# Performance work log

Measured on AMD Instinct MI355X. Metric: run time of the kernel, lower is better.

## Reference

```python
import jax, jax.numpy as jnp
import numpy as np

B, T, D, H = 4, 2048, 1024, 16
HD = D // H
K = 4            # templates per token
VOCAB = 32000


def setup_inputs() -> dict:
    key = jax.random.key(0)
    ks = jax.random.split(key, 6)
    x = jax.random.normal(ks[0], (B, T, D), dtype=jnp.float32)
    sequences = jax.random.randint(ks[1], (B, T, K), 0, VOCAB, dtype=jnp.int64)
    # xavier-uniform-ish scaled weights (torch Linear stores [out, in])
    Wqkv = jax.random.normal(ks[2], (3 * D, D), dtype=jnp.float32) * (1.0 / np.sqrt(D))
    Wout = jax.random.normal(ks[3], (D, D), dtype=jnp.float32) * (1.0 / np.sqrt(D))
    bout = jnp.zeros((D,), dtype=jnp.float32)
    emb = jax.random.normal(ks[4], (VOCAB, D), dtype=jnp.float32) * 0.02
    bias_scale = jnp.asarray(0.1, dtype=jnp.float32)
    return {"x": x, "sequences": sequences, "Wqkv": Wqkv, "Wout": Wout,
            "bout": bout, "emb": emb, "bias_scale": bias_scale}


def reference(x, sequences, Wqkv, Wout, bout, emb, bias_scale):
    b, t, d = x.shape
    h, hd = H, d // H
    # qkv projection (no bias): [B,T,3,H,hd]
    qkv = (x @ Wqkv.T).reshape(b, t, 3, h, hd)
    q = jnp.moveaxis(qkv[:, :, 0], 2, 1)  # [B,H,T,hd]
    k = jnp.moveaxis(qkv[:, :, 1], 2, 1)
    v = jnp.moveaxis(qkv[:, :, 2], 2, 1)
    scale = hd ** -0.5
    scores = jnp.einsum('bhqd,bhkd->bhqk', q, k) * scale  # [B,H,T,T]
    causal = jnp.tril(jnp.ones((t, t), dtype=bool))
    scores = jnp.where(causal[None, None], scores, -jnp.inf)
    w = jax.nn.softmax(scores, axis=-1)
    # dropout p=0.0 -> identity (eval-mode faithful)
    out = jnp.einsum('bhqk,bhkd->bhqd', w, v)
    out = jnp.moveaxis(out, 1, 2).reshape(b, t, d)
    # bias injection: sum template embeddings over template axis
    out = out + emb[sequences].sum(axis=-2) * bias_scale
    return out @ Wout.T + bout
```

## Files before the change

### kernel.cpp

```cpp
#include <hip/hip_runtime.h>
#include <stdint.h>


typedef __attribute__((ext_vector_type(8))) short s16x8;
typedef __attribute__((ext_vector_type(4))) short s16x4;
typedef __attribute__((ext_vector_type(4))) float f32x4;

static __device__ __forceinline__ unsigned short f32_bf16(float f) {
  union { float f; unsigned u; } v; v.f = f;
  unsigned r = v.u + 0x7fffu + ((v.u >> 16) & 1u);
  return (unsigned short)(r >> 16);
}
static __device__ __forceinline__ float bf16_f32(unsigned short h) {
  union { float f; unsigned u; } v; v.u = ((unsigned)h) << 16;
  return v.f;
}

__global__ __launch_bounds__(256) void cvt_f32_bf16_k(
    const float* __restrict__ in, unsigned short* __restrict__ out, int n8) {
  int i = blockIdx.x * 256 + threadIdx.x;
  if (i >= n8) return;
  const float4* p = (const float4*)(in + (long)i * 8);
  float4 a = p[0], b = p[1];
  s16x8 o;
  o[0] = (short)f32_bf16(a.x); o[1] = (short)f32_bf16(a.y);
  o[2] = (short)f32_bf16(a.z); o[3] = (short)f32_bf16(a.w);
  o[4] = (short)f32_bf16(b.x); o[5] = (short)f32_bf16(b.y);
  o[6] = (short)f32_bf16(b.z); o[7] = (short)f32_bf16(b.w);
  *(s16x8*)(out + (long)i * 8) = o;
}

__device__ __forceinline__ void glds16(const void* g, void* l) {
  __builtin_amdgcn_global_load_lds(
      (const __attribute__((address_space(1))) void*)g,
      (__attribute__((address_space(3))) void*)l, 16, 0, 0);
}

template <int OUTMODE>
__global__ __launch_bounds__(256) void gemm_bt(
    const unsigned short* __restrict__ A,
    const unsigned short* __restrict__ Bm,
    void* __restrict__ C0, void* __restrict__ C1, void* __restrict__ C2,
    const float* __restrict__ bias, int M, int N, int K) {
  __shared__ unsigned short Asl[128 * 32];
  __shared__ unsigned short Bsl[128 * 32];
  const int tid = threadIdx.x;
  const int l = tid & 63;
  const int w = tid >> 6;
  const int wr = w >> 1, wc = w & 1;
  const int bm = blockIdx.y, bn = blockIdx.x;

  f32x4 acc[4][4] = {};

  const unsigned short* Ag = A + (long)(bm * 128 + w * 16 + (l >> 2)) * K + (l & 3) * 8;
  const unsigned short* Bg = Bm + (long)(bn * 128 + w * 16 + (l >> 2)) * K + (l & 3) * 8;
  unsigned short* Al0 = &Asl[w * 512];
  unsigned short* Bl0 = &Bsl[w * 512];
  const int ro = (l & 15) * 32 + (l >> 4) * 8;

  for (int k0 = 0; k0 < K; k0 += 32) {
    __syncthreads();
    glds16(Ag + k0, Al0);
    glds16(Ag + 64 * K + k0, Al0 + 2048);
    glds16(Bg + k0, Bl0);
    glds16(Bg + 64 * K + k0, Bl0 + 2048);
    __syncthreads();
    s16x8 af[4], bfr[4];
#pragma unroll
    for (int i = 0; i < 4; ++i)
      af[i] = *(const s16x8*)&Asl[(wr * 64 + i * 16) * 32 + ro];
#pragma unroll
    for (int j = 0; j < 4; ++j)
      bfr[j] = *(const s16x8*)&Bsl[(wc * 64 + j * 16) * 32 + ro];
#pragma unroll
    for (int i = 0; i < 4; ++i)
#pragma unroll
      for (int j = 0; j < 4; ++j)
        acc[i][j] = __builtin_amdgcn_mfma_f32_16x16x32_bf16(af[i], bfr[j], acc[i][j], 0, 0, 0);
  }

  const int crow = bm * 128 + wr * 64 + (l >> 4) * 4;
  if (OUTMODE == 2) {
    unsigned short* C = (unsigned short*)(bn < 8 ? C0 : (bn < 16 ? C1 : C2));
    const int colb = (bn & 7) * 128 + wc * 64 + (l & 15);
#pragma unroll
    for (int i = 0; i < 4; ++i)
#pragma unroll
      for (int j = 0; j < 4; ++j)
#pragma unroll
        for (int r = 0; r < 4; ++r)
          C[(long)(crow + i * 16 + r) * 1024 + colb + j * 16] = f32_bf16(acc[i][j][r]);
  } else {
    float* C = (float*)C0;
    const int ccol = bn * 128 + wc * 64 + (l & 15);
#pragma unroll
    for (int i = 0; i < 4; ++i)
#pragma unroll
      for (int j = 0; j < 4; ++j) {
        float bv = bias[ccol + j * 16];
#pragma unroll
        for (int r = 0; r < 4; ++r)
          C[(long)(crow + i * 16 + r) * N + ccol + j * 16] = acc[i][j][r] + bv;
      }
  }
}


__device__ __forceinline__ void attn_tile(
    const unsigned short* __restrict__ Ksl, const unsigned short* __restrict__ Vtl,
    unsigned short* Psl, const s16x8* qf, f32x4* o, float* m, float* lsum,
    int qt0, int kv0, bool diag, int w, int g, int d15) {
  f32x4 s[4] = {};
#pragma unroll
  for (int st = 0; st < 4; ++st)
#pragma unroll
    for (int kc = 0; kc < 2; ++kc) {
      s16x8 kf = *(const s16x8*)&Ksl[(st * 16 + d15) * 72 + kc * 32 + g * 8];
      s[st] = __builtin_amdgcn_mfma_f32_16x16x32_bf16(qf[kc], kf, s[st], 0, 0, 0);
    }
#pragma unroll
  for (int r = 0; r < 4; ++r) {
    const int qabs = qt0 + w * 16 + g * 4 + r;
    float sv0 = s[0][r] * 0.125f, sv1 = s[1][r] * 0.125f;
    float sv2 = s[2][r] * 0.125f, sv3 = s[3][r] * 0.125f;
    if (diag) {
      if (kv0 + d15 > qabs) sv0 = -1e30f;
      if (kv0 + 16 + d15 > qabs) sv1 = -1e30f;
      if (kv0 + 32 + d15 > qabs) sv2 = -1e30f;
      if (kv0 + 48 + d15 > qabs) sv3 = -1e30f;
    }
    float mx = fmaxf(fmaxf(sv0, sv1), fmaxf(sv2, sv3));
    mx = fmaxf(mx, __shfl_xor(mx, 1));
    mx = fmaxf(mx, __shfl_xor(mx, 2));
    mx = fmaxf(mx, __shfl_xor(mx, 4));
    mx = fmaxf(mx, __shfl_xor(mx, 8));
    const float mn = fmaxf(m[r], mx);
    const float c = __expf(m[r] - mn);
    m[r] = mn;
    const float p0 = __expf(sv0 - mn), p1 = __expf(sv1 - mn);
    const float p2 = __expf(sv2 - mn), p3 = __expf(sv3 - mn);
    unsigned short* pr = &Psl[(w * 16 + g * 4 + r) * 72 + d15];
    pr[0] = f32_bf16(p0); pr[16] = f32_bf16(p1);
    pr[32] = f32_bf16(p2); pr[48] = f32_bf16(p3);
    float rsum = (p0 + p1) + (p2 + p3);
    rsum += __shfl_xor(rsum, 1);
    rsum += __shfl_xor(rsum, 2);
    rsum += __shfl_xor(rsum, 4);
    rsum += __shfl_xor(rsum, 8);
    lsum[r] = lsum[r] * c + rsum;
#pragma unroll
    for (int ct = 0; ct < 4; ++ct) o[ct][r] *= c;
  }
#pragma unroll
  for (int kc2 = 0; kc2 < 2; ++kc2) {
    s16x8 pf = *(const s16x8*)&Psl[(w * 16 + d15) * 72 + kc2 * 32 + g * 8];
#pragma unroll
    for (int ct = 0; ct < 4; ++ct) {
      s16x8 vf = *(const s16x8*)&Vtl[(ct * 16 + d15) * 72 + ((kc2 * 32 + g * 8) ^ (ct * 8))];
      o[ct] = __builtin_amdgcn_mfma_f32_16x16x32_bf16(pf, vf, o[ct], 0, 0, 0);
    }
  }
}

__global__ __launch_bounds__(256) void attn_k(
    const unsigned short* __restrict__ Qb, const unsigned short* __restrict__ Kb,
    const unsigned short* __restrict__ Vb, unsigned short* __restrict__ attn) {
  __shared__ unsigned short Ksl[64 * 72];
  __shared__ unsigned short Vtl[64 * 72];
  __shared__ unsigned short Psl[64 * 72];
  const int tid = threadIdx.x;
  const int l = tid & 63;
  const int w = tid >> 6;
  const int g = l >> 4;
  const int d15 = l & 15;
  const int bx = blockIdx.x;
  const int bh = blockIdx.y;
  const int b = bh >> 4, h = bh & 15;
  const int tok0 = b * 2048;
  const int qA = bx, qB = 31 - bx;
  const int nA = qA + 1, ntiles = qB + 1;
  const unsigned short* Qp = Qb + (long)tok0 * 1024 + h * 64;
  const unsigned short* Kp = Kb + (long)tok0 * 1024 + h * 64;
  const unsigned short* Vp = Vb + (long)tok0 * 1024 + h * 64;

  s16x8 qfA[2], qfB[2];
  {
    const unsigned short* qa = Qp + (long)(qA * 64 + w * 16 + d15) * 1024 + g * 8;
    qfA[0] = *(const s16x8*)qa;
    qfA[1] = *(const s16x8*)(qa + 32);
    const unsigned short* qbp = Qp + (long)(qB * 64 + w * 16 + d15) * 1024 + g * 8;
    qfB[0] = *(const s16x8*)qbp;
    qfB[1] = *(const s16x8*)(qbp + 32);
  }
  f32x4 oA[4] = {}, oB[4] = {};
  float mA[4], lA[4], mB[4], lB[4];
#pragma unroll
  for (int r = 0; r < 4; ++r) {
    mA[r] = -1e30f; lA[r] = 0.f; mB[r] = -1e30f; lB[r] = 0.f;
  }

  const int rs_ = tid >> 2;
  const int c0 = (tid & 3) * 16;
  const int vswz = rs_ ^ ((c0 >> 4) * 8);
  const unsigned short* Kg = Kp + (long)rs_ * 1024 + c0;
  const unsigned short* Vg = Vp + (long)rs_ * 1024 + c0;
  s16x8 kp0 = *(const s16x8*)Kg, kp1 = *(const s16x8*)(Kg + 8);
  s16x8 vp0 = *(const s16x8*)Vg, vp1 = *(const s16x8*)(Vg + 8);

  for (int it = 0; it < ntiles; ++it) {
    __syncthreads();
    *(s16x8*)&Ksl[rs_ * 72 + c0] = kp0;
    *(s16x8*)&Ksl[rs_ * 72 + c0 + 8] = kp1;
#pragma unroll
    for (int e = 0; e < 8; ++e) {
      Vtl[(c0 + e) * 72 + vswz] = (unsigned short)vp0[e];
      Vtl[(c0 + 8 + e) * 72 + vswz] = (unsigned short)vp1[e];
    }
    if (it + 1 < ntiles) {
      Kg += 65536; Vg += 65536;
      kp0 = *(const s16x8*)Kg; kp1 = *(const s16x8*)(Kg + 8);
      vp0 = *(const s16x8*)Vg; vp1 = *(const s16x8*)(Vg + 8);
    }
    __syncthreads();
    attn_tile(Ksl, Vtl, Psl, qfB, oB, mB, lB, qB * 64, it * 64, it == qB, w, g, d15);
    if (it < nA)
      attn_tile(Ksl, Vtl, Psl, qfA, oA, mA, lA, qA * 64, it * 64, it == qA, w, g, d15);
  }

  unsigned short* apB = attn + (long)(tok0 + qB * 64 + w * 16 + g * 4) * 1024 + h * 64 + d15;
  unsigned short* apA = attn + (long)(tok0 + qA * 64 + w * 16 + g * 4) * 1024 + h * 64 + d15;
#pragma unroll
  for (int r = 0; r < 4; ++r) {
    const float invB = 1.0f / lB[r];
    const float invA = 1.0f / lA[r];
#pragma unroll
    for (int ct = 0; ct < 4; ++ct) {
      apB[(long)r * 1024 + ct * 16] = f32_bf16(oB[ct][r] * invB);
      apA[(long)r * 1024 + ct * 16] = f32_bf16(oA[ct][r] * invA);
    }
  }
}

__global__ __launch_bounds__(256) void gather_add_k(
    unsigned short* __restrict__ attn, const int* __restrict__ seq,
    const float* __restrict__ emb, const float* __restrict__ bsc) {
  const int t = blockIdx.x;
  const int d0 = threadIdx.x * 4;
  const float sc = bsc[0];
  const int s0 = seq[t * 4 + 0], s1 = seq[t * 4 + 1];
  const int s2 = seq[t * 4 + 2], s3 = seq[t * 4 + 3];
  float4 e0 = *(const float4*)(emb + (long)s0 * 1024 + d0);
  float4 e1 = *(const float4*)(emb + (long)s1 * 1024 + d0);
  float4 e2 = *(const float4*)(emb + (long)s2 * 1024 + d0);
  float4 e3 = *(const float4*)(emb + (long)s3 * 1024 + d0);
  unsigned short* ap = attn + (long)t * 1024 + d0;
  s16x4 av = *(const s16x4*)ap;
  float r0 = bf16_f32((unsigned short)av[0]) + sc * (e0.x + e1.x + e2.x + e3.x);
  float r1 = bf16_f32((unsigned short)av[1]) + sc * (e0.y + e1.y + e2.y + e3.y);
  float r2 = bf16_f32((unsigned short)av[2]) + sc * (e0.z + e1.z + e2.z + e3.z);
  float r3 = bf16_f32((unsigned short)av[3]) + sc * (e0.w + e1.w + e2.w + e3.w);
  s16x4 ov;
  ov[0] = (short)f32_bf16(r0); ov[1] = (short)f32_bf16(r1);
  ov[2] = (short)f32_bf16(r2); ov[3] = (short)f32_bf16(r3);
  *(s16x4*)ap = ov;
}

extern "C" void kernel_launch(void* const* d_in, const int* in_sizes, int n_in,
                              void* d_out, int out_size, void* d_ws, size_t ws_size,
                              hipStream_t stream) {
  const float* x = (const float*)d_in[0];
  const int* seq = (const int*)d_in[1];
  const float* Wqkv = (const float*)d_in[2];
  const float* Wout = (const float*)d_in[3];
  const float* bout = (const float*)d_in[4];
  const float* emb = (const float*)d_in[5];
  const float* bsc = (const float*)d_in[6];

  uint8_t* ws = (uint8_t*)d_ws;
  unsigned short* xbf = (unsigned short*)ws;
  unsigned short* wqkvb = (unsigned short*)(ws + 16777216);
  unsigned short* woutb = (unsigned short*)(ws + 23068672);
  unsigned short* Qb = (unsigned short*)(ws + 25165824);
  unsigned short* Kb = (unsigned short*)d_out;
  unsigned short* Vb = Kb + (long)8192 * 1024;

  cvt_f32_bf16_k<<<4096, 256, 0, stream>>>(x, xbf, 1048576);
  cvt_f32_bf16_k<<<1536, 256, 0, stream>>>(Wqkv, wqkvb, 393216);
  cvt_f32_bf16_k<<<512, 256, 0, stream>>>(Wout, woutb, 131072);

  gemm_bt<2><<<dim3(24, 64), 256, 0, stream>>>(xbf, wqkvb, Qb, Kb, Vb, nullptr,
                                               8192, 3072, 1024);
  attn_k<<<dim3(16, 64), 256, 0, stream>>>(Qb, Kb, Vb, xbf);
  gather_add_k<<<8192, 256, 0, stream>>>(xbf, seq, emb, bsc);
  gemm_bt<1><<<dim3(8, 64), 256, 0, stream>>>(xbf, woutb, d_out, nullptr, nullptr,
                                              bout, 8192, 1024, 1024);
}
```

Baseline: 475.8 us.

## Fuse embedding gather into attention epilogue, fold softmax scale into Q, use exp2

Removes the separate gather_add kernel and instead adds the summed template embeddings inside the attention epilogue, so the attention output is not written, re-read and rewritten. The 1/sqrt(hd)*log2(e) factor is folded into Q during the QKV GEMM store, which lets the softmax use native exp2 without a per-score multiply. Row sums are kept per lane and reduced with shuffles only once at the end, and s_setprio raises wave priority around the MFMA sections. The epilogue's embedding gathers are scattered 4-byte loads per lane, which coalesce less well than the old float4 kernel. Rounding Q to bf16 after scaling also changes numerics slightly.

```diff
diff --git a/kernel.cpp b/kernel.cpp
--- a/kernel.cpp
+++ b/kernel.cpp
@@ -14,6 +14,13 @@
 static __device__ __forceinline__ float bf16_f32(unsigned short h) {
   union { float f; unsigned u; } v; v.u = ((unsigned)h) << 16;
   return v.f;
+}
+static __device__ __forceinline__ float fexp2(float x) {
+#if __has_builtin(__builtin_amdgcn_exp2f)
+  return __builtin_amdgcn_exp2f(x);
+#else
+  return exp2f(x);
+#endif
 }
 
 __global__ __launch_bounds__(256) void cvt_f32_bf16_k(
@@ -82,6 +89,7 @@
   const int crow = bm * 128 + wr * 64 + (l >> 4) * 4;
   if (OUTMODE == 2) {
     unsigned short* C = (unsigned short*)(bn < 8 ? C0 : (bn < 16 ? C1 : C2));
+    const float qsc = (bn < 8) ? 0.18033688f : 1.0f;
     const int colb = (bn & 7) * 128 + wc * 64 + (l & 15);
 #pragma unroll
     for (int i = 0; i < 4; ++i)
@@ -89,7 +97,7 @@
       for (int j = 0; j < 4; ++j)
 #pragma unroll
         for (int r = 0; r < 4; ++r)
-          C[(long)(crow + i * 16 + r) * 1024 + colb + j * 16] = f32_bf16(acc[i][j][r]);
+          C[(long)(crow + i * 16 + r) * 1024 + colb + j * 16] = f32_bf16(acc[i][j][r] * qsc);
   } else {
     float* C = (float*)C0;
     const int ccol = bn * 128 + wc * 64 + (l & 15);
@@ -108,9 +116,10 @@
 
 __device__ __forceinline__ void attn_tile(
     const unsigned short* __restrict__ Ksl, const unsigned short* __restrict__ Vtl,
-    unsigned short* Psl, const s16x8* qf, f32x4* o, float* m, float* lsum,
+    unsigned short* Psl, const s16x8* qf, f32x4* o, float* m, float* lpart,
     int qt0, int kv0, bool diag, int w, int g, int d15) {
   f32x4 s[4] = {};
+  __builtin_amdgcn_s_setprio(1);
 #pragma unroll
   for (int st = 0; st < 4; ++st)
 #pragma unroll
@@ -118,11 +127,11 @@
       s16x8 kf = *(const s16x8*)&Ksl[(st * 16 + d15) * 72 + kc * 32 + g * 8];
       s[st] = __builtin_amdgcn_mfma_f32_16x16x32_bf16(qf[kc], kf, s[st], 0, 0, 0);
     }
+  __builtin_amdgcn_s_setprio(0);
 #pragma unroll
   for (int r = 0; r < 4; ++r) {
     const int qabs = qt0 + w * 16 + g * 4 + r;
-    float sv0 = s[0][r] * 0.125f, sv1 = s[1][r] * 0.125f;
-    float sv2 = s[2][r] * 0.125f, sv3 = s[3][r] * 0.125f;
+    float sv0 = s[0][r], sv1 = s[1][r], sv2 = s[2][r], sv3 = s[3][r];
     if (diag) {
       if (kv0 + d15 > qabs) sv0 = -1e30f;
       if (kv0 + 16 + d15 > qabs) sv1 = -1e30f;
@@ -135,22 +144,18 @@
     mx = fmaxf(mx, __shfl_xor(mx, 4));
     mx = fmaxf(mx, __shfl_xor(mx, 8));
     const float mn = fmaxf(m[r], mx);
-    const float c = __expf(m[r] - mn);
+    const float c = fexp2(m[r] - mn);
     m[r] = mn;
-    const float p0 = __expf(sv0 - mn), p1 = __expf(sv1 - mn);
-    const float p2 = __expf(sv2 - mn), p3 = __expf(sv3 - mn);
+    const float p0 = fexp2(sv0 - mn), p1 = fexp2(sv1 - mn);
+    const float p2 = fexp2(sv2 - mn), p3 = fexp2(sv3 - mn);
     unsigned short* pr = &Psl[(w * 16 + g * 4 + r) * 72 + d15];
     pr[0] = f32_bf16(p0); pr[16] = f32_bf16(p1);
     pr[32] = f32_bf16(p2); pr[48] = f32_bf16(p3);
-    float rsum = (p0 + p1) + (p2 + p3);
-    rsum += __shfl_xor(rsum, 1);
-    rsum += __shfl_xor(rsum, 2);
-    rsum += __shfl_xor(rsum, 4);
-    rsum += __shfl_xor(rsum, 8);
-    lsum[r] = lsum[r] * c + rsum;
+    lpart[r] = lpart[r] * c + ((p0 + p1) + (p2 + p3));
 #pragma unroll
     for (int ct = 0; ct < 4; ++ct) o[ct][r] *= c;
   }
+  __builtin_amdgcn_s_setprio(1);
 #pragma unroll
   for (int kc2 = 0; kc2 < 2; ++kc2) {
     s16x8 pf = *(const s16x8*)&Psl[(w * 16 + d15) * 72 + kc2 * 32 + g * 8];
@@ -160,11 +165,14 @@
       o[ct] = __builtin_amdgcn_mfma_f32_16x16x32_bf16(pf, vf, o[ct], 0, 0, 0);
     }
   }
+  __builtin_amdgcn_s_setprio(0);
 }
 
 __global__ __launch_bounds__(256) void attn_k(
     const unsigned short* __restrict__ Qb, const unsigned short* __restrict__ Kb,
-    const unsigned short* __restrict__ Vb, unsigned short* __restrict__ attn) {
+    const unsigned short* __restrict__ Vb, unsigned short* __restrict__ attn,
+    const int* __restrict__ seq, const float* __restrict__ emb,
+    const float* __restrict__ bsc) {
   __shared__ unsigned short Ksl[64 * 72];
   __shared__ unsigned short Vtl[64 * 72];
   __shared__ unsigned short Psl[64 * 72];
@@ -227,42 +235,45 @@
       attn_tile(Ksl, Vtl, Psl, qfA, oA, mA, lA, qA * 64, it * 64, it == qA, w, g, d15);
   }
 
-  unsigned short* apB = attn + (long)(tok0 + qB * 64 + w * 16 + g * 4) * 1024 + h * 64 + d15;
-  unsigned short* apA = attn + (long)(tok0 + qA * 64 + w * 16 + g * 4) * 1024 + h * 64 + d15;
+#pragma unroll
+  for (int r = 0; r < 4; ++r) {
+    float sB = lB[r], sA = lA[r];
+    sB += __shfl_xor(sB, 1); sB += __shfl_xor(sB, 2);
+    sB += __shfl_xor(sB, 4); sB += __shfl_xor(sB, 8);
+    sA += __shfl_xor(sA, 1); sA += __shfl_xor(sA, 2);
+    sA += __shfl_xor(sA, 4); sA += __shfl_xor(sA, 8);
+    lB[r] = sB; lA[r] = sA;
+  }
+
+  const float sc = bsc[0];
+  const int colbase = h * 64 + d15;
+  const int tB0 = tok0 + qB * 64 + w * 16 + g * 4;
+  const int tA0 = tok0 + qA * 64 + w * 16 + g * 4;
+  unsigned short* apB = attn + (long)tB0 * 1024 + colbase;
+  unsigned short* apA = attn + (long)tA0 * 1024 + colbase;
 #pragma unroll
   for (int r = 0; r < 4; ++r) {
     const float invB = 1.0f / lB[r];
     const float invA = 1.0f / lA[r];
+    const int* sqB = seq + (long)(tB0 + r) * 4;
+    const int* sqA = seq + (long)(tA0 + r) * 4;
+    const float* eB0 = emb + (long)sqB[0] * 1024 + colbase;
+    const float* eB1 = emb + (long)sqB[1] * 1024 + colbase;
+    const float* eB2 = emb + (long)sqB[2] * 1024 + colbase;
+    const float* eB3 = emb + (long)sqB[3] * 1024 + colbase;
+    const float* eA0 = emb + (long)sqA[0] * 1024 + colbase;
+    const float* eA1 = emb + (long)sqA[1] * 1024 + colbase;
+    const float* eA2 = emb + (long)sqA[2] * 1024 + colbase;
+    const float* eA3 = emb + (long)sqA[3] * 1024 + colbase;
 #pragma unroll
     for (int ct = 0; ct < 4; ++ct) {
-      apB[(long)r * 1024 + ct * 16] = f32_bf16(oB[ct][r] * invB);
-      apA[(long)r * 1024 + ct * 16] = f32_bf16(oA[ct][r] * invA);
-    }
-  }
-}
-
-__global__ __launch_bounds__(256) void gather_add_k(
-    unsigned short* __restrict__ attn, const int* __restrict__ seq,
-    const float* __restrict__ emb, const float* __restrict__ bsc) {
-  const int t = blockIdx.x;
-  const int d0 = threadIdx.x * 4;
-  const float sc = bsc[0];
-  const int s0 = seq[t * 4 + 0], s1 = seq[t * 4 + 1];
-  const int s2 = seq[t * 4 + 2], s3 = seq[t * 4 + 3];
-  float4 e0 = *(const float4*)(emb + (long)s0 * 1024 + d0);
-  float4 e1 = *(const float4*)(emb + (long)s1 * 1024 + d0);
-  float4 e2 = *(const float4*)(emb + (long)s2 * 1024 + d0);
-  float4 e3 = *(const float4*)(emb + (long)s3 * 1024 + d0);
-  unsigned short* ap = attn + (long)t * 1024 + d0;
-  s16x4 av = *(const s16x4*)ap;
-  float r0 = bf16_f32((unsigned short)av[0]) + sc * (e0.x + e1.x + e2.x + e3.x);
-  float r1 = bf16_f32((unsigned short)av[1]) + sc * (e0.y + e1.y + e2.y + e3.y);
-  float r2 = bf16_f32((unsigned short)av[2]) + sc * (e0.z + e1.z + e2.z + e3.z);
-  float r3 = bf16_f32((unsigned short)av[3]) + sc * (e0.w + e1.w + e2.w + e3.w);
-  s16x4 ov;
-  ov[0] = (short)f32_bf16(r0); ov[1] = (short)f32_bf16(r1);
-  ov[2] = (short)f32_bf16(r2); ov[3] = (short)f32_bf16(r3);
-  *(s16x4*)ap = ov;
+      const int cc = ct * 16;
+      float embB = (eB0[cc] + eB1[cc]) + (eB2[cc] + eB3[cc]);
+      float embA = (eA0[cc] + eA1[cc]) + (eA2[cc] + eA3[cc]);
+      apB[(long)r * 1024 + cc] = f32_bf16(oB[ct][r] * invB + sc * embB);
+      apA[(long)r * 1024 + cc] = f32_bf16(oA[ct][r] * invA + sc * embA);
+    }
+  }
 }
 
 extern "C" void kernel_launch(void* const* d_in, const int* in_sizes, int n_in,
@@ -290,8 +301,7 @@
 
   gemm_bt<2><<<dim3(24, 64), 256, 0, stream>>>(xbf, wqkvb, Qb, Kb, Vb, nullptr,
                                                8192, 3072, 1024);
-  attn_k<<<dim3(16, 64), 256, 0, stream>>>(Qb, Kb, Vb, xbf);
-  gather_add_k<<<8192, 256, 0, stream>>>(xbf, seq, emb, bsc);
+  attn_k<<<dim3(16, 64), 256, 0, stream>>>(Qb, Kb, Vb, xbf, seq, emb, bsc);
   gemm_bt<1><<<dim3(8, 64), 256, 0, stream>>>(xbf, woutb, d_out, nullptr, nullptr,
                                               bout, 8192, 1024, 1024);
 }
```

After: 435.3 us. 8.5% less time.
